# Performance work log

Hardware: AMD Instinct MI355X
Metric: run time of the kernel (lower is better)

## Reference

```python
import jax, jax.numpy as jnp
import numpy as np

N, IN_CAPS, IN_LEN = 32, 1152, 32
OUT_CAPS, OUT_LEN = 64, 32
NUM_ITERATIONS = 3


def setup_inputs() -> dict:
    key = jax.random.key(0)
    k1, k2 = jax.random.split(key)
    x = jax.random.normal(k1, (N, IN_CAPS, IN_LEN), dtype=jnp.float32)
    # learnable weight, torch.randn init: (out_capsules, out_length, in_length)
    weight = jax.random.normal(k2, (OUT_CAPS, OUT_LEN, IN_LEN), dtype=jnp.float32)
    return {"x": x, "weight": weight}


def _squash(v):
    # v * ||v|| / (1 + ||v||^2)  ==  (||v||^2/(1+||v||^2)) * v/||v||
    norm_sq = jnp.sum(v * v, axis=-1, keepdims=True)
    norm = jnp.sqrt(norm_sq)
    return v * norm / (1.0 + norm_sq)


def reference(x, weight):
    # priors u_hat: [N, out_caps, in_caps, out_len]
    priors = jnp.einsum('oli,bni->bonl', weight, x)
    logits = jnp.zeros_like(priors)
    output = None
    for r in range(NUM_ITERATIONS):
        # coupling coefficients: softmax over output capsules (axis=1)
        probs = jax.nn.softmax(logits, axis=1)
        # weighted sum over input capsules -> [N, out_caps, 1, out_len]
        output = jnp.sum(probs * priors, axis=-2, keepdims=True)
        if r != NUM_ITERATIONS - 1:
            output = _squash(output)
            # agreement update: [N, out_caps, in_caps, 1]
            logits = logits + jnp.sum(priors * output, axis=-1, keepdims=True)
    output = _squash(output)  # squash=True default
    return jnp.squeeze(output, axis=-2)  # [N, out_caps, out_len]
```

## Files before the change

### kernel.cpp

```cpp
#include <hip/hip_runtime.h>
#include <math.h>


#define N_B      32
#define IN_CAPS  1152
#define IN_LEN   32
#define OUT_CAPS 64
#define OUT_LEN  32

#define NCHUNK 16
#define NPB    (IN_CAPS / NCHUNK)
#define PASS_WAVES 4
#define NPW    (NPB / PASS_WAVES)

__global__ __launch_bounds__(256) void k_init(const float* __restrict__ x,
                                              const float* __restrict__ W,
                                              float* __restrict__ T) {
    const int b   = blockIdx.x;
    const int tid = threadIdx.x;
    const float* xb = x + (size_t)b * IN_CAPS * IN_LEN;

    __shared__ float4 red4[32][8];
    {
        const int q = tid & 7;
        const int g = tid >> 3;
        float4 acc = make_float4(0.f, 0.f, 0.f, 0.f);
        for (int n = g; n < IN_CAPS; n += 32) {
            const float4 v = *(const float4*)(xb + n * IN_LEN + q * 4);
            acc.x += v.x; acc.y += v.y; acc.z += v.z; acc.w += v.w;
        }
        red4[g][q] = acc;
    }
    __syncthreads();
    __shared__ float s0[IN_LEN];
    if (tid < 8) {
        float4 v = make_float4(0.f, 0.f, 0.f, 0.f);
        for (int g = 0; g < 32; ++g) {
            const float4 r = red4[g][tid];
            v.x += r.x; v.y += r.y; v.z += r.z; v.w += r.w;
        }
        const float inv = 1.f / 64.f;
        s0[tid * 4 + 0] = v.x * inv;
        s0[tid * 4 + 1] = v.y * inv;
        s0[tid * 4 + 2] = v.z * inv;
        s0[tid * 4 + 3] = v.w * inv;
    }
    __syncthreads();

    __shared__ float u[OUT_CAPS * OUT_LEN];
    for (int e = tid; e < OUT_CAPS * OUT_LEN; e += 256) {
        const float* wrow = W + (size_t)e * IN_LEN;
        float a = 0.f;
#pragma unroll
        for (int i = 0; i < IN_LEN; ++i) a = fmaf(wrow[i], s0[i], a);
        u[e] = a;
    }
    __syncthreads();

    __shared__ float scale[OUT_CAPS];
    if (tid < OUT_CAPS) {
        float ns = 0.f;
#pragma unroll
        for (int l = 0; l < OUT_LEN; ++l) { const float v = u[tid * OUT_LEN + l]; ns = fmaf(v, v, ns); }
        scale[tid] = sqrtf(ns) / (1.f + ns);
    }
    __syncthreads();

    for (int e = tid; e < OUT_CAPS * IN_LEN; e += 256) {
        const int o = e >> 5, i = e & 31;
        float a = 0.f;
#pragma unroll
        for (int l = 0; l < OUT_LEN; ++l)
            a = fmaf(W[((size_t)o * OUT_LEN + l) * IN_LEN + i], u[o * OUT_LEN + l], a);
        T[(size_t)b * OUT_CAPS * IN_LEN + e] = a * scale[o];
    }
}

__global__ __launch_bounds__(256) void k_pass(const float* __restrict__ x,
                                              const float* __restrict__ T,
                                              float* __restrict__ part) {
    const int b    = blockIdx.x >> 4;
    const int c    = blockIdx.x & (NCHUNK - 1);
    const int lane = threadIdx.x & 63;
    const int wave = __builtin_amdgcn_readfirstlane(threadIdx.x >> 6);

    float t[IN_LEN], s[IN_LEN];
    {
        const float* Trow = T + ((size_t)b * OUT_CAPS + lane) * IN_LEN;
#pragma unroll
        for (int i = 0; i < IN_LEN; ++i) { t[i] = Trow[i]; s[i] = 0.f; }
    }

    const float* xb = x + ((size_t)b * IN_CAPS + c * NPB + wave * NPW) * IN_LEN;
    for (int j = 0; j < NPW; ++j) {
        const float* xn = xb + j * IN_LEN;
        float xv[IN_LEN];
#pragma unroll
        for (int i = 0; i < IN_LEN; ++i) xv[i] = xn[i];

        float logit = 0.f;
#pragma unroll
        for (int i = 0; i < IN_LEN; ++i) logit = fmaf(xv[i], t[i], logit);

        float m = logit;
#pragma unroll
        for (int off = 32; off >= 1; off >>= 1) m = fmaxf(m, __shfl_xor(m, off, 64));
        const float p = __expf(logit - m);
        float sum = p;
#pragma unroll
        for (int off = 32; off >= 1; off >>= 1) sum += __shfl_xor(sum, off, 64);
        const float prob = p / sum;

#pragma unroll
        for (int i = 0; i < IN_LEN; ++i) s[i] = fmaf(prob, xv[i], s[i]);
    }

    __shared__ __align__(16) float sp[PASS_WAVES * OUT_CAPS * IN_LEN];
    {
        float4* dst = (float4*)&sp[(wave * OUT_CAPS + lane) * IN_LEN];
#pragma unroll
        for (int q = 0; q < 8; ++q)
            dst[q] = make_float4(s[4 * q], s[4 * q + 1], s[4 * q + 2], s[4 * q + 3]);
    }
    __syncthreads();
    {
        const float4* sp4 = (const float4*)sp;
        float4* pb4 = (float4*)(part + ((size_t)b * NCHUNK + c) * OUT_CAPS * IN_LEN);
        for (int e = threadIdx.x; e < OUT_CAPS * IN_LEN / 4; e += 256) {
            const float4 a0 = sp4[e];
            const float4 a1 = sp4[512 + e];
            const float4 a2 = sp4[1024 + e];
            const float4 a3 = sp4[1536 + e];
            pb4[e] = make_float4(a0.x + a1.x + a2.x + a3.x,
                                 a0.y + a1.y + a2.y + a3.y,
                                 a0.z + a1.z + a2.z + a3.z,
                                 a0.w + a1.w + a2.w + a3.w);
        }
    }
}

__global__ __launch_bounds__(256) void k_vt(const float* __restrict__ W,
                                            const float* __restrict__ part,
                                            float* __restrict__ T,
                                            float* __restrict__ out,
                                            int final_iter) {
    const int b   = blockIdx.x;
    const int tid = threadIdx.x;

    __shared__ float s_lds[OUT_CAPS * IN_LEN];
    {
        const float4* pb4 = (const float4*)(part + (size_t)b * NCHUNK * OUT_CAPS * IN_LEN);
        for (int e = tid; e < OUT_CAPS * IN_LEN / 4; e += 256) {
            float4 acc = make_float4(0.f, 0.f, 0.f, 0.f);
#pragma unroll
            for (int c = 0; c < NCHUNK; ++c) {
                const float4 v = pb4[c * (OUT_CAPS * IN_LEN / 4) + e];
                acc.x += v.x; acc.y += v.y; acc.z += v.z; acc.w += v.w;
            }
            ((float4*)s_lds)[e] = acc;
        }
    }
    __syncthreads();

    __shared__ float u[OUT_CAPS * OUT_LEN];
    for (int e = tid; e < OUT_CAPS * OUT_LEN; e += 256) {
        const int o = e >> 5;
        const float* wrow = W + (size_t)e * IN_LEN;
        const float* srow = s_lds + o * IN_LEN;
        float a = 0.f;
#pragma unroll
        for (int i = 0; i < IN_LEN; ++i) a = fmaf(wrow[i], srow[i], a);
        u[e] = a;
    }
    __syncthreads();

    __shared__ float scale[OUT_CAPS];
    if (tid < OUT_CAPS) {
        float ns = 0.f;
#pragma unroll
        for (int l = 0; l < OUT_LEN; ++l) { const float v = u[tid * OUT_LEN + l]; ns = fmaf(v, v, ns); }
        scale[tid] = sqrtf(ns) / (1.f + ns);
    }
    __syncthreads();

    if (final_iter) {
        for (int e = tid; e < OUT_CAPS * OUT_LEN; e += 256)
            out[(size_t)b * OUT_CAPS * OUT_LEN + e] = u[e] * scale[e >> 5];
    } else {
        for (int e = tid; e < OUT_CAPS * IN_LEN; e += 256) {
            const int o = e >> 5, i = e & 31;
            float a = 0.f;
#pragma unroll
            for (int l = 0; l < OUT_LEN; ++l)
                a = fmaf(W[((size_t)o * OUT_LEN + l) * IN_LEN + i], u[o * OUT_LEN + l], a);
            T[(size_t)b * OUT_CAPS * IN_LEN + e] += a * scale[o];
        }
    }
}

extern "C" void kernel_launch(void* const* d_in, const int* in_sizes, int n_in,
                              void* d_out, int out_size, void* d_ws, size_t ws_size,
                              hipStream_t stream) {
    const float* x = (const float*)d_in[0];
    const float* W = (const float*)d_in[1];
    float* out = (float*)d_out;

    float* T    = (float*)d_ws;
    float* part = T + (size_t)N_B * OUT_CAPS * IN_LEN;

    k_init<<<N_B, 256, 0, stream>>>(x, W, T);
    k_pass<<<N_B * NCHUNK, 256, 0, stream>>>(x, T, part);
    k_vt  <<<N_B, 256, 0, stream>>>(W, part, T, out, 0);
    k_pass<<<N_B * NCHUNK, 256, 0, stream>>>(x, T, part);
    k_vt  <<<N_B, 256, 0, stream>>>(W, part, T, out, 1);
}
```

Measured before the change: 140.5 us.

## Fuse reduction/update kernel into pass kernel via last-block atomic counter

Merges the per-batch reduction, squash and T update (former k_vt) into the tail of k_pass, with the last-arriving chunk block for each batch elected through an atomic counter and thread fences. This drops two kernel launches and their serialization gaps. The pass loop is also restructured to process two input capsules per iteration with float4 vectors, interleaving the two softmax shuffle reductions for more ILP. In exchange, counters must be reset in k_init, extra LDS is allocated in every pass block, and the tail work runs on only 32 blocks at the end of the pass.

After: 209.9 us. 49.4% more time.

```diff
diff --git a/kernel.cpp b/kernel.cpp
--- a/kernel.cpp
+++ b/kernel.cpp
@@ -7,26 +7,33 @@
 #define IN_LEN   32
 #define OUT_CAPS 64
 #define OUT_LEN  32
-
-#define NCHUNK 16
-#define NPB    (IN_CAPS / NCHUNK)
-#define PASS_WAVES 4
-#define NPW    (NPB / PASS_WAVES)
+#define NCHUNK   16
+#define NPB      (IN_CAPS / NCHUNK)
+#define NPW      (NPB / 4)
+
+__device__ __forceinline__ float4 f4fma(const float4 a, const float4 b, float4 c) {
+    c.x = fmaf(a.x, b.x, c.x); c.y = fmaf(a.y, b.y, c.y);
+    c.z = fmaf(a.z, b.z, c.z); c.w = fmaf(a.w, b.w, c.w);
+    return c;
+}
+__device__ __forceinline__ float f4hsum(const float4 a) { return (a.x + a.y) + (a.z + a.w); }
 
 __global__ __launch_bounds__(256) void k_init(const float* __restrict__ x,
                                               const float* __restrict__ W,
-                                              float* __restrict__ T) {
+                                              float* __restrict__ T,
+                                              int* __restrict__ cnt) {
     const int b   = blockIdx.x;
     const int tid = threadIdx.x;
     const float* xb = x + (size_t)b * IN_CAPS * IN_LEN;
 
+    if (tid < 2) cnt[tid * N_B + b] = 0;
+
     __shared__ float4 red4[32][8];
     {
-        const int q = tid & 7;
-        const int g = tid >> 3;
+        const int q = tid & 7, g = tid >> 3;
         float4 acc = make_float4(0.f, 0.f, 0.f, 0.f);
         for (int n = g; n < IN_CAPS; n += 32) {
-            const float4 v = *(const float4*)(xb + n * IN_LEN + q * 4);
+            const float4 v = ((const float4*)(xb + n * IN_LEN))[q];
             acc.x += v.x; acc.y += v.y; acc.z += v.z; acc.w += v.w;
         }
         red4[g][q] = acc;
@@ -49,11 +56,12 @@
 
     __shared__ float u[OUT_CAPS * OUT_LEN];
     for (int e = tid; e < OUT_CAPS * OUT_LEN; e += 256) {
-        const float* wrow = W + (size_t)e * IN_LEN;
-        float a = 0.f;
-#pragma unroll
-        for (int i = 0; i < IN_LEN; ++i) a = fmaf(wrow[i], s0[i], a);
-        u[e] = a;
+        const float4* wr = (const float4*)(W + (size_t)e * IN_LEN);
+        const float4* sr = (const float4*)s0;
+        float4 a4 = make_float4(0.f, 0.f, 0.f, 0.f);
+#pragma unroll
+        for (int q = 0; q < 8; ++q) a4 = f4fma(wr[q], sr[q], a4);
+        u[e] = f4hsum(a4);
     }
     __syncthreads();
 
@@ -71,129 +79,147 @@
         float a = 0.f;
 #pragma unroll
         for (int l = 0; l < OUT_LEN; ++l)
-            a = fmaf(W[((size_t)o * OUT_LEN + l) * IN_LEN + i], u[o * OUT_LEN + l], a);
+            a = fmaf(W[(size_t)(o * OUT_LEN + l) * IN_LEN + i], u[o * OUT_LEN + l], a);
         T[(size_t)b * OUT_CAPS * IN_LEN + e] = a * scale[o];
     }
 }
 
 __global__ __launch_bounds__(256) void k_pass(const float* __restrict__ x,
-                                              const float* __restrict__ T,
-                                              float* __restrict__ part) {
+                                              const float* __restrict__ W,
+                                              float* __restrict__ T,
+                                              float* __restrict__ part,
+                                              int* __restrict__ cnt,
+                                              float* __restrict__ out,
+                                              int phase) {
     const int b    = blockIdx.x >> 4;
     const int c    = blockIdx.x & (NCHUNK - 1);
-    const int lane = threadIdx.x & 63;
-    const int wave = __builtin_amdgcn_readfirstlane(threadIdx.x >> 6);
-
-    float t[IN_LEN], s[IN_LEN];
-    {
-        const float* Trow = T + ((size_t)b * OUT_CAPS + lane) * IN_LEN;
-#pragma unroll
-        for (int i = 0; i < IN_LEN; ++i) { t[i] = Trow[i]; s[i] = 0.f; }
-    }
-
-    const float* xb = x + ((size_t)b * IN_CAPS + c * NPB + wave * NPW) * IN_LEN;
-    for (int j = 0; j < NPW; ++j) {
-        const float* xn = xb + j * IN_LEN;
-        float xv[IN_LEN];
-#pragma unroll
-        for (int i = 0; i < IN_LEN; ++i) xv[i] = xn[i];
-
-        float logit = 0.f;
-#pragma unroll
-        for (int i = 0; i < IN_LEN; ++i) logit = fmaf(xv[i], t[i], logit);
-
-        float m = logit;
-#pragma unroll
-        for (int off = 32; off >= 1; off >>= 1) m = fmaxf(m, __shfl_xor(m, off, 64));
-        const float p = __expf(logit - m);
-        float sum = p;
-#pragma unroll
-        for (int off = 32; off >= 1; off >>= 1) sum += __shfl_xor(sum, off, 64);
-        const float prob = p / sum;
-
-#pragma unroll
-        for (int i = 0; i < IN_LEN; ++i) s[i] = fmaf(prob, xv[i], s[i]);
-    }
-
-    __shared__ __align__(16) float sp[PASS_WAVES * OUT_CAPS * IN_LEN];
-    {
-        float4* dst = (float4*)&sp[(wave * OUT_CAPS + lane) * IN_LEN];
-#pragma unroll
-        for (int q = 0; q < 8; ++q)
-            dst[q] = make_float4(s[4 * q], s[4 * q + 1], s[4 * q + 2], s[4 * q + 3]);
-    }
-    __syncthreads();
-    {
-        const float4* sp4 = (const float4*)sp;
-        float4* pb4 = (float4*)(part + ((size_t)b * NCHUNK + c) * OUT_CAPS * IN_LEN);
-        for (int e = threadIdx.x; e < OUT_CAPS * IN_LEN / 4; e += 256) {
-            const float4 a0 = sp4[e];
-            const float4 a1 = sp4[512 + e];
-            const float4 a2 = sp4[1024 + e];
-            const float4 a3 = sp4[1536 + e];
-            pb4[e] = make_float4(a0.x + a1.x + a2.x + a3.x,
-                                 a0.y + a1.y + a2.y + a3.y,
-                                 a0.z + a1.z + a2.z + a3.z,
-                                 a0.w + a1.w + a2.w + a3.w);
-        }
-    }
-}
-
-__global__ __launch_bounds__(256) void k_vt(const float* __restrict__ W,
-                                            const float* __restrict__ part,
-                                            float* __restrict__ T,
-                                            float* __restrict__ out,
-                                            int final_iter) {
-    const int b   = blockIdx.x;
-    const int tid = threadIdx.x;
-
-    __shared__ float s_lds[OUT_CAPS * IN_LEN];
-    {
-        const float4* pb4 = (const float4*)(part + (size_t)b * NCHUNK * OUT_CAPS * IN_LEN);
+    const int tid  = threadIdx.x;
+    const int lane = tid & 63;
+    const int wave = tid >> 6;
+
+    __shared__ __align__(16) float buf[4 * OUT_CAPS * IN_LEN];
+    __shared__ int is_last;
+
+    float4 t4[8], s4[8];
+    {
+        const float4* Trow = (const float4*)(T + ((size_t)b * OUT_CAPS + lane) * IN_LEN);
+#pragma unroll
+        for (int q = 0; q < 8; ++q) { t4[q] = Trow[q]; s4[q] = make_float4(0.f, 0.f, 0.f, 0.f); }
+    }
+
+    const float* xb = x + (size_t)(b * IN_CAPS + c * NPB + wave * NPW) * IN_LEN;
+    for (int j = 0; j < NPW; j += 2) {
+        const float4* x0 = (const float4*)(xb + j * IN_LEN);
+        const float4* x1 = (const float4*)(xb + (j + 1) * IN_LEN);
+        float4 xq[8], yq[8];
+#pragma unroll
+        for (int q = 0; q < 8; ++q) { xq[q] = x0[q]; yq[q] = x1[q]; }
+
+        float4 d0 = make_float4(0.f, 0.f, 0.f, 0.f);
+        float4 d1 = make_float4(0.f, 0.f, 0.f, 0.f);
+#pragma unroll
+        for (int q = 0; q < 8; ++q) { d0 = f4fma(xq[q], t4[q], d0); d1 = f4fma(yq[q], t4[q], d1); }
+        const float l0 = f4hsum(d0), l1 = f4hsum(d1);
+
+        float m0 = l0, m1 = l1;
+#pragma unroll
+        for (int off = 32; off >= 1; off >>= 1) {
+            m0 = fmaxf(m0, __shfl_xor(m0, off, 64));
+            m1 = fmaxf(m1, __shfl_xor(m1, off, 64));
+        }
+        const float e0 = __expf(l0 - m0), e1 = __expf(l1 - m1);
+        float z0 = e0, z1 = e1;
+#pragma unroll
+        for (int off = 32; off >= 1; off >>= 1) {
+            z0 += __shfl_xor(z0, off, 64);
+            z1 += __shfl_xor(z1, off, 64);
+        }
+        const float pr0 = e0 / z0, pr1 = e1 / z1;
+        const float4 p0v = make_float4(pr0, pr0, pr0, pr0);
+        const float4 p1v = make_float4(pr1, pr1, pr1, pr1);
+#pragma unroll
+        for (int q = 0; q < 8; ++q) {
+            s4[q] = f4fma(p0v, xq[q], s4[q]);
+            s4[q] = f4fma(p1v, yq[q], s4[q]);
+        }
+    }
+
+    {
+        float4* dst = (float4*)(buf + (size_t)(wave * OUT_CAPS + lane) * IN_LEN);
+#pragma unroll
+        for (int q = 0; q < 8; ++q) dst[q] = s4[q];
+    }
+    __syncthreads();
+    {
+        const float4* b4 = (const float4*)buf;
+        float4* pb4 = (float4*)(part + (size_t)(b * NCHUNK + c) * (OUT_CAPS * IN_LEN));
         for (int e = tid; e < OUT_CAPS * IN_LEN / 4; e += 256) {
-            float4 acc = make_float4(0.f, 0.f, 0.f, 0.f);
-#pragma unroll
-            for (int c = 0; c < NCHUNK; ++c) {
-                const float4 v = pb4[c * (OUT_CAPS * IN_LEN / 4) + e];
-                acc.x += v.x; acc.y += v.y; acc.z += v.z; acc.w += v.w;
+            float4 a = b4[e];
+            const float4 a1 = b4[512 + e], a2 = b4[1024 + e], a3 = b4[1536 + e];
+            a.x += a1.x + a2.x + a3.x;
+            a.y += a1.y + a2.y + a3.y;
+            a.z += a1.z + a2.z + a3.z;
+            a.w += a1.w + a2.w + a3.w;
+            pb4[e] = a;
+        }
+    }
+    __syncthreads();
+
+    if (tid == 0) {
+        __threadfence();
+        const int old = atomicAdd(&cnt[phase * N_B + b], 1);
+        is_last = (old == NCHUNK - 1) ? 1 : 0;
+    }
+    __syncthreads();
+    if (!is_last) return;
+    __threadfence();
+
+    __shared__ float s_l[OUT_CAPS * IN_LEN];
+    __shared__ float u_l[OUT_CAPS * OUT_LEN];
+    __shared__ float sc_l[OUT_CAPS];
+
+    {
+        const float4* pb = (const float4*)(part + (size_t)b * NCHUNK * (OUT_CAPS * IN_LEN));
+        for (int e = tid; e < OUT_CAPS * IN_LEN / 4; e += 256) {
+            float4 a = make_float4(0.f, 0.f, 0.f, 0.f);
+#pragma unroll
+            for (int cc = 0; cc < NCHUNK; ++cc) {
+                const float4 v = pb[cc * (OUT_CAPS * IN_LEN / 4) + e];
+                a.x += v.x; a.y += v.y; a.z += v.z; a.w += v.w;
             }
-            ((float4*)s_lds)[e] = acc;
-        }
-    }
-    __syncthreads();
-
-    __shared__ float u[OUT_CAPS * OUT_LEN];
+            ((float4*)s_l)[e] = a;
+        }
+    }
+    __syncthreads();
     for (int e = tid; e < OUT_CAPS * OUT_LEN; e += 256) {
         const int o = e >> 5;
-        const float* wrow = W + (size_t)e * IN_LEN;
-        const float* srow = s_lds + o * IN_LEN;
-        float a = 0.f;
-#pragma unroll
-        for (int i = 0; i < IN_LEN; ++i) a = fmaf(wrow[i], srow[i], a);
-        u[e] = a;
-    }
-    __syncthreads();
-
-    __shared__ float scale[OUT_CAPS];
+        const float4* wr = (const float4*)(W + (size_t)e * IN_LEN);
+        const float4* sr = (const float4*)(s_l + o * IN_LEN);
+        float4 a4 = make_float4(0.f, 0.f, 0.f, 0.f);
+#pragma unroll
+        for (int q = 0; q < 8; ++q) a4 = f4fma(wr[q], sr[q], a4);
+        u_l[e] = f4hsum(a4);
+    }
+    __syncthreads();
     if (tid < OUT_CAPS) {
         float ns = 0.f;
 #pragma unroll
-        for (int l = 0; l < OUT_LEN; ++l) { const float v = u[tid * OUT_LEN + l]; ns = fmaf(v, v, ns); }
-        scale[tid] = sqrtf(ns) / (1.f + ns);
-    }
-    __syncthreads();
-
-    if (final_iter) {
+        for (int l = 0; l < OUT_LEN; ++l) { const float v = u_l[tid * OUT_LEN + l]; ns = fmaf(v, v, ns); }
+        sc_l[tid] = sqrtf(ns) / (1.f + ns);
+    }
+    __syncthreads();
+
+    if (phase == 1) {
         for (int e = tid; e < OUT_CAPS * OUT_LEN; e += 256)
-            out[(size_t)b * OUT_CAPS * OUT_LEN + e] = u[e] * scale[e >> 5];
+            out[(size_t)b * (OUT_CAPS * OUT_LEN) + e] = u_l[e] * sc_l[e >> 5];
     } else {
         for (int e = tid; e < OUT_CAPS * IN_LEN; e += 256) {
             const int o = e >> 5, i = e & 31;
             float a = 0.f;
 #pragma unroll
             for (int l = 0; l < OUT_LEN; ++l)
-                a = fmaf(W[((size_t)o * OUT_LEN + l) * IN_LEN + i], u[o * OUT_LEN + l], a);
-            T[(size_t)b * OUT_CAPS * IN_LEN + e] += a * scale[o];
+                a = fmaf(W[(size_t)(o * OUT_LEN + l) * IN_LEN + i], u_l[o * OUT_LEN + l], a);
+            T[(size_t)b * OUT_CAPS * IN_LEN + e] += a * sc_l[o];
         }
     }
 }
@@ -207,10 +233,9 @@
 
     float* T    = (float*)d_ws;
     float* part = T + (size_t)N_B * OUT_CAPS * IN_LEN;
-
-    k_init<<<N_B, 256, 0, stream>>>(x, W, T);
-    k_pass<<<N_B * NCHUNK, 256, 0, stream>>>(x, T, part);
-    k_vt  <<<N_B, 256, 0, stream>>>(W, part, T, out, 0);
-    k_pass<<<N_B * NCHUNK, 256, 0, stream>>>(x, T, part);
-    k_vt  <<<N_B, 256, 0, stream>>>(W, part, T, out, 1);
-}
+    int*   cnt  = (int*)(part + (size_t)N_B * NCHUNK * OUT_CAPS * IN_LEN);
+
+    k_init<<<N_B, 256, 0, stream>>>(x, W, T, cnt);
+    k_pass<<<N_B * NCHUNK, 256, 0, stream>>>(x, W, T, part, cnt, out, 0);
+    k_pass<<<N_B * NCHUNK, 256, 0, stream>>>(x, W, T, part, cnt, out, 1);
+}
```
